# Kernel optimization log

Hardware: AMD Instinct MI355X
Metric: run time of the kernel (lower is better)

The kernel has to match this reference:

```python
import jax, jax.numpy as jnp
from jax import lax
import numpy as np


def _conv(x, w, b, stride=1, pad=0):
    # x: NCHW, w: OIHW
    o = lax.conv_general_dilated(x, w, (stride, stride), [(pad, pad), (pad, pad)],
                                 dimension_numbers=('NCHW', 'OIHW', 'NCHW'))
    return o + b[None, :, None, None]


def _up2(x):
    return jnp.repeat(jnp.repeat(x, 2, axis=2), 2, axis=3)


def _boundary_agg(x, w, b):
    # up_to_bottom = prefix-max along H; bottom_to_up = suffix-max along H;
    # left_to_right / right_to_left (via rot90) = prefix/suffix max along W (square spatial).
    x1 = lax.cummax(x, axis=2)
    x2 = lax.cummax(x, axis=2, reverse=True)
    x3 = lax.cummax(x, axis=3)
    x4 = lax.cummax(x, axis=3, reverse=True)
    return _conv(jnp.concatenate([x, x1, x2, x3, x4], axis=1), w, b)


def _forward(C3, C4, C5,
             ba3_w, ba3_b, ba4_w, ba4_b, ba5_w, ba5_b,
             p5_1_w, p5_1_b, p5_1d_w, p5_1d_b, p5_2_w, p5_2_b,
             p4_1_w, p4_1_b, p4_1d_w, p4_1d_b, p4_2_w, p4_2_b,
             p3_1_w, p3_1_b, p3_1d_w, p3_1d_b, p3_2_w, p3_2_b,
             p6_w, p6_b, p7_w, p7_b,
             c34_w, c34_b, c45_w, c45_b, c35_w, c35_b,
             gamma3, gamma4, gamma5):
    C3_BA = _boundary_agg(C3, ba3_w, ba3_b)
    C4_BA = _boundary_agg(C4, ba4_w, ba4_b)
    C5_BA = _boundary_agg(C5, ba5_w, ba5_b)
    # top-down path
    P5 = _conv(C5, p5_1_w, p5_1_b)
    P5u1 = _up2(P5)
    P5u2 = _up2(P5u1)
    P5 = _conv(P5, p5_2_w, p5_2_b, 1, 1)
    P4 = _conv(C4, p4_1_w, p4_1_b) + P5u1
    P4u1 = _up2(P4)
    P4 = _conv(P4, p4_2_w, p4_2_b, 1, 1)
    P3 = _conv(C3, p3_1_w, p3_1_b) + P4u1 + P5u2
    P3 = _conv(P3, p3_2_w, p3_2_b, 1, 1)
    # bottom-up (dual) path on boundary-aggregated features
    P3d = _conv(C3_BA, p3_1d_w, p3_1d_b)
    P3d1 = _conv(P3d, c34_w, c34_b, 2, 1)   # 3x3 s2 p1
    P3d2 = _conv(P3d1, c35_w, c35_b, 2, 0)  # 2x2 s2 p0
    P4d = _conv(C4_BA, p4_1d_w, p4_1d_b) + P3d1
    P4d1 = _conv(P4d, c45_w, c45_b, 2, 0)   # 2x2 s2 p0
    P5d = _conv(C5_BA, p5_1d_w, p5_1d_b) + P4d1 + P3d2
    # extra levels
    P6 = _conv(C5, p6_w, p6_b, 2, 1)
    P7 = _conv(jax.nn.relu(P6), p7_w, p7_b, 2, 1)
    # gated merge
    O3 = gamma3 * P3d + (1.0 - gamma3) * P3
    O4 = gamma4 * P4d + (1.0 - gamma4) * P4
    O5 = gamma5 * P5d + (1.0 - gamma5) * P5
    return (O3, O4, O5, P6, P7)


def setup_inputs() -> dict:
    key = jax.random.key(0)
    ks = iter(jax.random.split(key, 48))
    def rnd(shape, scale):
        return jax.random.normal(next(ks), shape, dtype=jnp.float32) * scale
    B, F = 8, 256
    d = {
        'C3': rnd((B, 256, 64, 64), 1.0),
        'C4': rnd((B, 512, 32, 32), 1.0),
        'C5': rnd((B, 1024, 16, 16), 1.0),
        # Boundary_Aggregation 1x1 convs: in_channels*5 -> in_channels
        'ba3_w': rnd((256, 1280, 1, 1), 0.02), 'ba3_b': rnd((256,), 0.02),
        'ba4_w': rnd((512, 2560, 1, 1), 0.02), 'ba4_b': rnd((512,), 0.02),
        'ba5_w': rnd((1024, 5120, 1, 1), 0.01), 'ba5_b': rnd((1024,), 0.02),
        # FPN lateral / smoothing convs
        'p5_1_w': rnd((F, 1024, 1, 1), 0.02), 'p5_1_b': rnd((F,), 0.02),
        'p5_1d_w': rnd((F, 1024, 1, 1), 0.02), 'p5_1d_b': rnd((F,), 0.02),
        'p5_2_w': rnd((F, F, 3, 3), 0.02), 'p5_2_b': rnd((F,), 0.02),
        'p4_1_w': rnd((F, 512, 1, 1), 0.02), 'p4_1_b': rnd((F,), 0.02),
        'p4_1d_w': rnd((F, 512, 1, 1), 0.02), 'p4_1d_b': rnd((F,), 0.02),
        'p4_2_w': rnd((F, F, 3, 3), 0.02), 'p4_2_b': rnd((F,), 0.02),
        'p3_1_w': rnd((F, 256, 1, 1), 0.02), 'p3_1_b': rnd((F,), 0.02),
        'p3_1d_w': rnd((F, 256, 1, 1), 0.02), 'p3_1d_b': rnd((F,), 0.02),
        'p3_2_w': rnd((F, F, 3, 3), 0.02), 'p3_2_b': rnd((F,), 0.02),
        'p6_w': rnd((F, 1024, 3, 3), 0.02), 'p6_b': rnd((F,), 0.02),
        'p7_w': rnd((F, F, 3, 3), 0.02), 'p7_b': rnd((F,), 0.02),
        # downsample convs in dual path
        'c34_w': rnd((F, F, 3, 3), 0.02), 'c34_b': rnd((F,), 0.02),
        'c45_w': rnd((F, F, 2, 2), 0.02), 'c45_b': rnd((F,), 0.02),
        'c35_w': rnd((F, F, 2, 2), 0.02), 'c35_b': rnd((F,), 0.02),
        'gamma3': rnd((1,), 0.3), 'gamma4': rnd((1,), 0.3), 'gamma5': rnd((1,), 0.3),
    }
    return d


def reference(C3, C4, C5,
              ba3_w, ba3_b, ba4_w, ba4_b, ba5_w, ba5_b,
              p5_1_w, p5_1_b, p5_1d_w, p5_1d_b, p5_2_w, p5_2_b,
              p4_1_w, p4_1_b, p4_1d_w, p4_1d_b, p4_2_w, p4_2_b,
              p3_1_w, p3_1_b, p3_1d_w, p3_1d_b, p3_2_w, p3_2_b,
              p6_w, p6_b, p7_w, p7_b,
              c34_w, c34_b, c45_w, c45_b, c35_w, c35_b,
              gamma3, gamma4, gamma5):
    return _forward(C3, C4, C5,
                    ba3_w, ba3_b, ba4_w, ba4_b, ba5_w, ba5_b,
                    p5_1_w, p5_1_b, p5_1d_w, p5_1d_b, p5_2_w, p5_2_b,
                    p4_1_w, p4_1_b, p4_1d_w, p4_1d_b, p4_2_w, p4_2_b,
                    p3_1_w, p3_1_b, p3_1d_w, p3_1d_b, p3_2_w, p3_2_b,
                    p6_w, p6_b, p7_w, p7_b,
                    c34_w, c34_b, c45_w, c45_b, c35_w, c35_b,
                    gamma3, gamma4, gamma5)
```

## Files before the change

kernel.cpp:

```cpp
#include <hip/hip_runtime.h>

typedef unsigned short u16;
typedef __attribute__((ext_vector_type(8))) short s8v;
typedef __attribute__((ext_vector_type(4))) float f4v;

__device__ __forceinline__ u16 f2bf(float f) {
  unsigned int x = __float_as_uint(f);
  return (u16)((x + 0x7fffu + ((x >> 16) & 1u)) >> 16);
}
__device__ __forceinline__ float bf2f(u16 u) {
  return __uint_as_float(((unsigned int)u) << 16);
}
__device__ __forceinline__ void gload16(const void* g, void* l) {
  __builtin_amdgcn_global_load_lds(
      (const __attribute__((address_space(1))) void*)g,
      (__attribute__((address_space(3))) void*)l, 16, 0, 0);
}

struct Epi {
  const float* bias;
  const u16* r1; int r1Hp, r1pad, r1sh;
  const u16* r2; int r2Hp, r2pad, r2sh;
  const float* gamma; const u16* other; int oHp, opad, gmode;
  u16* outB; int oBHp, oBpad, oBrelu;
  float* outF;
};

__device__ __forceinline__ size_t nhwc_idx(int b, int h, int w, int Hp, int pad, int Cc, int m) {
  return (((size_t)(b * Hp + h + pad)) * Hp + (w + pad)) * Cc + m;
}

__device__ __forceinline__ f4v epi_val(f4v a, int mbase, int b, int oh, int ow,
                                       float g, const Epi& ep) {
  float v[4];
#pragma unroll
  for (int r = 0; r < 4; ++r) v[r] = a[r];
  if (ep.bias) {
    const float* bp = &ep.bias[mbase];
#pragma unroll
    for (int r = 0; r < 4; ++r) v[r] += bp[r];
  }
  if (ep.r1) {
    const u16* rp = &ep.r1[nhwc_idx(b, oh >> ep.r1sh, ow >> ep.r1sh, ep.r1Hp, ep.r1pad, 256, mbase)];
#pragma unroll
    for (int r = 0; r < 4; ++r) v[r] += bf2f(rp[r]);
  }
  if (ep.r2) {
    const u16* rp = &ep.r2[nhwc_idx(b, oh >> ep.r2sh, ow >> ep.r2sh, ep.r2Hp, ep.r2pad, 256, mbase)];
#pragma unroll
    for (int r = 0; r < 4; ++r) v[r] += bf2f(rp[r]);
  }
  if (ep.gmode) {
    const u16* op = &ep.other[nhwc_idx(b, oh, ow, ep.oHp, ep.opad, 256, mbase)];
#pragma unroll
    for (int r = 0; r < 4; ++r) {
      float o = bf2f(op[r]);
      v[r] = (ep.gmode == 1) ? (g * o + (1.f - g) * v[r]) : (g * v[r] + (1.f - g) * o);
    }
  }
  f4v out;
#pragma unroll
  for (int r = 0; r < 4; ++r) out[r] = v[r];
  return out;
}

__device__ __forceinline__ void epi_storeB(f4v v, int mbase, int b, int oh, int ow,
                                           int M, const Epi& ep) {
  u16* obp = &ep.outB[nhwc_idx(b, oh, ow, ep.oBHp, ep.oBpad, M, mbase)];
  ushort4 pk;
  if (ep.oBrelu) { pk.x = f2bf(fmaxf(v[0], 0.f)); pk.y = f2bf(fmaxf(v[1], 0.f));
                   pk.z = f2bf(fmaxf(v[2], 0.f)); pk.w = f2bf(fmaxf(v[3], 0.f)); }
  else { pk.x = f2bf(v[0]); pk.y = f2bf(v[1]); pk.z = f2bf(v[2]); pk.w = f2bf(v[3]); }
  *(ushort4*)obp = pk;
}

__device__ __forceinline__ void epi4(f4v a, int mbase, int b, int oh, int ow,
                                     int p, int M, int l2ohow, float g, const Epi& ep) {
  f4v v = epi_val(a, mbase, b, oh, ow, g, ep);
  if (ep.outF) {
    float* fp = &ep.outF[(((size_t)(b * M + mbase)) << l2ohow) + p];
#pragma unroll
    for (int r = 0; r < 4; ++r) fp[(size_t)r << l2ohow] = v[r];
  }
  if (ep.outB) epi_storeB(v, mbase, b, oh, ow, M, ep);
}

struct WSeg { const float* src; u16* dst; int K, l2Cin, mode, ktiles, blk0; };
struct WTab { WSeg s[17]; };

__global__ __launch_bounds__(256) void k_cvt_w(WTab tab) {
  int bid = blockIdx.x;
  int si = 0;
#pragma unroll
  for (int i = 1; i < 17; ++i) si += (bid >= tab.s[i].blk0) ? 1 : 0;
  WSeg sg = tab.s[si];
  int rel = bid - sg.blk0;
  int m = rel / sg.ktiles;
  int kt = rel - m * sg.ktiles;
  int r = kt * 256 + threadIdx.x;
  if (r >= sg.K) return;
  int Cin = 1 << sg.l2Cin;
  int q = r >> sg.l2Cin, c = r & (Cin - 1);
  int sidx;
  if (sg.mode == 1) {
    int og = (q < 4) ? (q + 1) : 0;
    sidx = m * sg.K + og * Cin + c;
  } else {
    int KHW = sg.K >> sg.l2Cin;
    sidx = (m * Cin + c) * KHW + q;
  }
  sg.dst[(size_t)m * sg.K + r] = f2bf(sg.src[sidx]);
}

__global__ __launch_bounds__(256) void k_cvt_x(const float* __restrict__ in, u16* __restrict__ out,
                                               int C, int H, int W, int Hp, int P, int tw) {
  __shared__ u16 tile[32][33];
  const int t = threadIdx.x;
  const int b = blockIdx.z, h = blockIdx.y;
  const int tc = blockIdx.x / tw, twi = blockIdx.x - tc * tw;
  const int c0 = tc * 32, w0 = twi * 32;
#pragma unroll
  for (int r = 0; r < 4; ++r) {
    int cl = (t >> 5) * 4 + r, wl = t & 31;
    if (w0 + wl < W) tile[cl][wl] = f2bf(in[(((size_t)b * C + c0 + cl) * H + h) * W + w0 + wl]);
  }
  __syncthreads();
#pragma unroll
  for (int r = 0; r < 4; ++r) {
    int wl = (t >> 5) * 4 + r, cl = t & 31;
    if (w0 + wl < W) out[(((size_t)(b * Hp + h + P)) * Hp + (w0 + wl + P)) * C + c0 + cl] = tile[cl][wl];
  }
}

__global__ __launch_bounds__(256)
void k_scanH(const u16* __restrict__ in, u16* __restrict__ out0, u16* __restrict__ out1,
             int S, int C) {
  const int cpw = C >> 2;
  const int wpb = 256 / cpw;
  const int strips = S / wpb;
  const int t = threadIdx.x;
  const int wl = t / cpw, c4 = t - wl * cpw;
  const int bb = blockIdx.x / strips, strip = blockIdx.x - bb * strips;
  const int w = strip * wpb + wl;
  const size_t hstr = (size_t)S * C;
  const size_t base = (((size_t)bb * S) * S + w) * C + c4 * 4;
  float m0 = -INFINITY, m1 = -INFINITY, m2 = -INFINITY, m3 = -INFINITY;
  if (blockIdx.y == 0) {
    for (int h = 0; h < S; ++h) {
      ushort4 v = *(const ushort4*)&in[base + (size_t)h * hstr];
      m0 = fmaxf(m0, bf2f(v.x)); m1 = fmaxf(m1, bf2f(v.y));
      m2 = fmaxf(m2, bf2f(v.z)); m3 = fmaxf(m3, bf2f(v.w));
      ushort4 o; o.x = f2bf(m0); o.y = f2bf(m1); o.z = f2bf(m2); o.w = f2bf(m3);
      *(ushort4*)&out0[base + (size_t)h * hstr] = o;
    }
  } else {
    for (int h = S - 1; h >= 0; --h) {
      ushort4 v = *(const ushort4*)&in[base + (size_t)h * hstr];
      m0 = fmaxf(m0, bf2f(v.x)); m1 = fmaxf(m1, bf2f(v.y));
      m2 = fmaxf(m2, bf2f(v.z)); m3 = fmaxf(m3, bf2f(v.w));
      ushort4 o; o.x = f2bf(m0); o.y = f2bf(m1); o.z = f2bf(m2); o.w = f2bf(m3);
      *(ushort4*)&out1[base + (size_t)h * hstr] = o;
    }
  }
}

__global__ __launch_bounds__(256)
void k_scanW(const u16* __restrict__ in, u16* __restrict__ out0, u16* __restrict__ out1,
             int S, int C) {
  const int cph = C >> 2;
  const int hpb = 256 / cph;
  const int strips = S / hpb;
  const int t = threadIdx.x;
  const int hl = t / cph, c4 = t - hl * cph;
  const int bb = blockIdx.x / strips, strip = blockIdx.x - bb * strips;
  const int h = strip * hpb + hl;
  const size_t wstr = (size_t)C;
  const size_t base = (((size_t)bb * S + h) * S) * C + c4 * 4;
  float m0 = -INFINITY, m1 = -INFINITY, m2 = -INFINITY, m3 = -INFINITY;
  if (blockIdx.y == 0) {
    for (int w = 0; w < S; ++w) {
      ushort4 v = *(const ushort4*)&in[base + (size_t)w * wstr];
      m0 = fmaxf(m0, bf2f(v.x)); m1 = fmaxf(m1, bf2f(v.y));
      m2 = fmaxf(m2, bf2f(v.z)); m3 = fmaxf(m3, bf2f(v.w));
      ushort4 o; o.x = f2bf(m0); o.y = f2bf(m1); o.z = f2bf(m2); o.w = f2bf(m3);
      *(ushort4*)&out0[base + (size_t)w * wstr] = o;
    }
  } else {
    for (int w = S - 1; w >= 0; --w) {
      ushort4 v = *(const ushort4*)&in[base + (size_t)w * wstr];
      m0 = fmaxf(m0, bf2f(v.x)); m1 = fmaxf(m1, bf2f(v.y));
      m2 = fmaxf(m2, bf2f(v.z)); m3 = fmaxf(m3, bf2f(v.w));
      ushort4 o; o.x = f2bf(m0); o.y = f2bf(m1); o.z = f2bf(m2); o.w = f2bf(m3);
      *(ushort4*)&out1[base + (size_t)w * wstr] = o;
    }
  }
}

template<int QDIV, int KW, int STR, bool FUSE>
__global__ __launch_bounds__(256)
void k_gemm(const u16* __restrict__ X, const u16* __restrict__ X2,
            const u16* __restrict__ Wt,
            float* __restrict__ part, int C, int l2C, int Hp, int ipad,
            int l2ohow, int l2ow, int K, int Ksp, int M, int N, Epi ep) {
  __shared__ __align__(16) u16 SMEM[FUSE ? 12288 : 17408];
  u16* Al = SMEM;
  u16* Bl = SMEM + 4096;
  float* Cl = (float*)SMEM;
  const int tid = threadIdx.x, lane = tid & 63, wid = tid >> 6;

  int ntile, mtile;
  {
    const int NT = gridDim.x, MT = gridDim.y;
    int nm = blockIdx.x + NT * blockIdx.y;
    if ((NT & 7) == 0) {
      int low = nm & 7, r = nm >> 3;
      mtile = r % MT;
      ntile = ((r / MT) << 3) + low;
    } else { ntile = blockIdx.x; mtile = blockIdx.y; }
  }
  const int n0 = ntile * 128, m0 = mtile * 64;
  const int kb = blockIdx.z * Ksp;
  const int mw = (wid >> 1) * 32, nw = (wid & 1) * 64;

  const int srow = lane >> 2;
  const int schunk = (lane & 3) ^ ((srow >> 1) & 3);

  const u16* pa0 = Wt + (size_t)(m0 + wid * 16 + srow) * K + kb + schunk * 8;

  const u16* pb0 = nullptr; const u16* pb1 = nullptr;
  int rowB[2], ohsB[2], owsB[2];
  int q = 0, cnt = 0, khs = 0, kws = 0;
#pragma unroll
  for (int j = 0; j < 2; ++j) {
    int n = n0 + wid * 32 + j * 16 + srow;
    int b = n >> l2ohow, p = n & ((1 << l2ohow) - 1);
    int oh = p >> l2ow, ow = p & ((1 << l2ow) - 1);
    if (QDIV == 1) {
      const u16* gg = X + ((size_t)(b * Hp + oh + ipad) * Hp + (ow + ipad)) * C + kb + schunk * 8;
      if (j == 0) pb0 = gg; else pb1 = gg;
    } else if (QDIV == 5) {
      rowB[j] = n;
    } else {
      rowB[j] = b * Hp; ohsB[j] = oh * STR + ipad; owsB[j] = ow * STR + ipad;
    }
  }
  if (QDIV == 5) {
    q = kb >> l2C;
    int c0 = kb & (C - 1);
    cnt = (C - c0) >> 5;
    const u16* base = (q < 4) ? (X + (((size_t)q << Hp) << l2C)) : X2;
    pb0 = base + (((size_t)rowB[0]) << l2C) + c0 + schunk * 8;
    pb1 = base + (((size_t)rowB[1]) << l2C) + c0 + schunk * 8;
  } else if (QDIV != 1) {
    q = kb >> l2C;
    int c0 = kb & (C - 1);
    cnt = (C - c0) >> 5;
    if (QDIV == 4) { khs = q >> 1; kws = q & 1; } else { khs = q / 3; kws = q - khs * 3; }
    pb0 = X + ((size_t)(rowB[0] + ohsB[0] + khs) * Hp + (owsB[0] + kws)) * C + c0 + schunk * 8;
    pb1 = X + ((size_t)(rowB[1] + ohsB[1] + khs) * Hp + (owsB[1] + kws)) * C + c0 + schunk * 8;
  }

  f4v acc[2][4];
#pragma unroll
  for (int i = 0; i < 2; ++i)
#pragma unroll
    for (int j = 0; j < 4; ++j) acc[i][j] = (f4v){0.f, 0.f, 0.f, 0.f};

  const int fr = lane & 15, kc = lane >> 4;
  const int fxor = (kc ^ ((fr >> 1) & 3)) * 8;

  auto advB = [&]() {
    if (QDIV == 1) { pb0 += 32; pb1 += 32; }
    else if (--cnt == 0) {
      ++q; cnt = C >> 5;
      if (QDIV == 5) {
        const u16* base = (q < 4) ? (X + (((size_t)q << Hp) << l2C)) : X2;
        pb0 = base + (((size_t)rowB[0]) << l2C) + schunk * 8;
        pb1 = base + (((size_t)rowB[1]) << l2C) + schunk * 8;
      } else {
        if (++kws == KW) { kws = 0; ++khs; }
        pb0 = X + ((size_t)(rowB[0] + ohsB[0] + khs) * Hp + (owsB[0] + kws)) * C + schunk * 8;
        pb1 = X + ((size_t)(rowB[1] + ohsB[1] + khs) * Hp + (owsB[1] + kws)) * C + schunk * 8;
      }
    } else { pb0 += 32; pb1 += 32; }
  };
  auto stage = [&](int buf) {
    u16* la = Al + buf * 2048 + wid * 512;
    u16* lb = Bl + buf * 4096 + wid * 1024;
    gload16(pa0, la);
    gload16(pb0, lb); gload16(pb1, lb + 512);
    pa0 += 32;
    advB();
  };

  const int nt = Ksp >> 5;
  stage(0);
  for (int t = 0; t < nt; ++t) {
    const int cur = t & 1;
    if (t + 1 < nt) {
      stage(cur ^ 1);
      asm volatile("s_waitcnt vmcnt(3)" ::: "memory");
    } else {
      asm volatile("s_waitcnt vmcnt(0)" ::: "memory");
    }
    __builtin_amdgcn_s_barrier();
    asm volatile("" ::: "memory");
    const u16* ca = Al + cur * 2048;
    const u16* cb = Bl + cur * 4096;
    s8v a[2], bv[4];
#pragma unroll
    for (int mf = 0; mf < 2; ++mf) a[mf] = *(const s8v*)&ca[(mw + mf * 16 + fr) * 32 + fxor];
#pragma unroll
    for (int nf = 0; nf < 4; ++nf) bv[nf] = *(const s8v*)&cb[(nw + nf * 16 + fr) * 32 + fxor];
#pragma unroll
    for (int mf = 0; mf < 2; ++mf)
#pragma unroll
      for (int nf = 0; nf < 4; ++nf)
        acc[mf][nf] = __builtin_amdgcn_mfma_f32_16x16x32_bf16(a[mf], bv[nf], acc[mf][nf], 0, 0, 0);
    __builtin_amdgcn_s_barrier();
    asm volatile("" ::: "memory");
  }

  const int r4 = kc * 4;
  if (FUSE) {
    float g = ep.gmode ? *ep.gamma : 0.f;
#pragma unroll
    for (int nf = 0; nf < 4; ++nf) {
      int n = n0 + nw + nf * 16 + fr;
      int b = n >> l2ohow, p = n & ((1 << l2ohow) - 1);
      int oh = p >> l2ow, ow = p & ((1 << l2ow) - 1);
#pragma unroll
      for (int mf = 0; mf < 2; ++mf)
        epi4(acc[mf][nf], m0 + mw + mf * 16 + r4, b, oh, ow, p, M, l2ohow, g, ep);
    }
  } else {
#pragma unroll
    for (int nf = 0; nf < 4; ++nf) {
      int pl = nw + nf * 16 + fr;
#pragma unroll
      for (int mf = 0; mf < 2; ++mf)
        *(f4v*)&Cl[pl * 68 + mw + mf * 16 + r4] = acc[mf][nf];
    }
    __builtin_amdgcn_s_barrier();
    asm volatile("" ::: "memory");
    const int ml2 = (tid & 15) << 2;
    const int prow = tid >> 4;
#pragma unroll
    for (int pass = 0; pass < 8; ++pass) {
      int pl = pass * 16 + prow;
      int n = n0 + pl;
      *(f4v*)&part[((size_t)blockIdx.z * N + n) * M + m0 + ml2] =
          *(const f4v*)&Cl[pl * 68 + ml2];
    }
  }
}

__global__ __launch_bounds__(256)
void k_red2(const float* __restrict__ part, int z, int l2N, int l2M4, int M,
            int l2ohow, int l2ow, Epi ep) {
  const size_t total = (size_t)1 << (l2N + l2M4);
  const int N = 1 << l2N;
  float g = ep.gmode ? *ep.gamma : 0.f;
  for (size_t t = (size_t)blockIdx.x * 256 + threadIdx.x; t < total;
       t += (size_t)gridDim.x * 256) {
    int m4 = (int)(t & ((1u << l2M4) - 1));
    int n = (int)(t >> l2M4);
    int m = m4 << 2;
    f4v v = (f4v){0.f, 0.f, 0.f, 0.f};
    for (int s = 0; s < z; ++s) {
      f4v x = *(const f4v*)&part[((size_t)s * N + n) * M + m];
      v = v + x;
    }
    int b = n >> l2ohow, p = n & ((1 << l2ohow) - 1);
    int oh = p >> l2ow, ow = p & ((1 << l2ow) - 1);
    epi4(v, m, b, oh, ow, p, M, l2ohow, g, ep);
  }
}

static const size_t WR_BA3 = 0, WR_BA4 = 327680, WR_BA5 = 1638400,
  WR_P51 = 6881280, WR_P51D = 7143424, WR_P52 = 7405568, WR_P41 = 7995392,
  WR_P41D = 8126464, WR_P42 = 8257536, WR_P31 = 8847360, WR_P31D = 8912896,
  WR_P32 = 8978432, WR_P6 = 9568256, WR_P7 = 11927552, WR_C34 = 12517376,
  WR_C45 = 13107200, WR_C35 = 13369344;
static const size_t O_C3N = 13631488, O_C4N = 22020096, O_C5N = 26214400,
  O_C3BA = 28311552, O_C4BA = 36700160, O_C5BA = 40894464,
  O_CAT = 42991616, O_SCR = 76546048;
static const size_t O_P3D = O_CAT, O_P3PRE = O_CAT + 8921088,
  O_P4PRE = O_CAT + 17842176, O_P3D1 = O_CAT + 20209664,
  O_P4D = O_CAT + 22306816, O_P4D1 = O_CAT + 24403968,
  O_P3D2 = O_CAT + 24928256, O_P5PRE = O_CAT + 25452544,
  O_P5S = O_CAT + 26116096, O_P6R = O_CAT + 26640384, O_C5P = O_CAT + 26845184;

extern "C" void kernel_launch(void* const* d_in, const int* in_sizes, int n_in,
                              void* d_out, int out_size, void* d_ws, size_t ws_size,
                              hipStream_t stream) {
  (void)in_sizes; (void)n_in; (void)out_size; (void)ws_size;
  const float* C3 = (const float*)d_in[0];
  const float* C4 = (const float*)d_in[1];
  const float* C5 = (const float*)d_in[2];
  const float* ba3_w = (const float*)d_in[3];  const float* ba3_b = (const float*)d_in[4];
  const float* ba4_w = (const float*)d_in[5];  const float* ba4_b = (const float*)d_in[6];
  const float* ba5_w = (const float*)d_in[7];  const float* ba5_b = (const float*)d_in[8];
  const float* p5_1_w = (const float*)d_in[9];  const float* p5_1_b = (const float*)d_in[10];
  const float* p5_1d_w = (const float*)d_in[11]; const float* p5_1d_b = (const float*)d_in[12];
  const float* p5_2_w = (const float*)d_in[13]; const float* p5_2_b = (const float*)d_in[14];
  const float* p4_1_w = (const float*)d_in[15]; const float* p4_1_b = (const float*)d_in[16];
  const float* p4_1d_w = (const float*)d_in[17]; const float* p4_1d_b = (const float*)d_in[18];
  const float* p4_2_w = (const float*)d_in[19]; const float* p4_2_b = (const float*)d_in[20];
  const float* p3_1_w = (const float*)d_in[21]; const float* p3_1_b = (const float*)d_in[22];
  const float* p3_1d_w = (const float*)d_in[23]; const float* p3_1d_b = (const float*)d_in[24];
  const float* p3_2_w = (const float*)d_in[25]; const float* p3_2_b = (const float*)d_in[26];
  const float* p6_w = (const float*)d_in[27]; const float* p6_b = (const float*)d_in[28];
  const float* p7_w = (const float*)d_in[29]; const float* p7_b = (const float*)d_in[30];
  const float* c34_w = (const float*)d_in[31]; const float* c34_b = (const float*)d_in[32];
  const float* c45_w = (const float*)d_in[33]; const float* c45_b = (const float*)d_in[34];
  const float* c35_w = (const float*)d_in[35]; const float* c35_b = (const float*)d_in[36];
  const float* g3 = (const float*)d_in[37];
  const float* g4 = (const float*)d_in[38];
  const float* g5 = (const float*)d_in[39];

  float* out = (float*)d_out;
  float* O3 = out;
  float* O4 = out + 8388608;
  float* O5 = out + 10485760;
  float* P6o = out + 11010048;
  float* P7o = out + 11141120;

  u16* wsu = (u16*)d_ws;
  u16* c3n = wsu + O_C3N;  u16* c4n = wsu + O_C4N;  u16* c5n = wsu + O_C5N;
  u16* c3ba = wsu + O_C3BA; u16* c4ba = wsu + O_C4BA; u16* c5ba = wsu + O_C5BA;
  u16* catb = wsu + O_CAT;
  u16* scr = wsu + O_SCR;
  u16* p3d = wsu + O_P3D;  u16* p3d1 = wsu + O_P3D1; u16* p3d2 = wsu + O_P3D2;
  u16* p4d = wsu + O_P4D;  u16* p4d1 = wsu + O_P4D1;
  u16* p5pre = wsu + O_P5PRE; u16* p5s = wsu + O_P5S; u16* p4pre = wsu + O_P4PRE;
  u16* p3pre = wsu + O_P3PRE; u16* p6r = wsu + O_P6R; u16* c5p = wsu + O_C5P;
  float* part = (float*)scr;
  float* partba = (float*)scr;

  const Epi enone = {nullptr, nullptr,0,0,0, nullptr,0,0,0, nullptr,nullptr,0,0,0, nullptr,0,0,0, nullptr};

  WTab tab;
  int ti = 0, blk = 0;
  auto add = [&](const float* s, size_t off, int M, int K, int l2Cin, int mode) {
    int kt = (K + 255) / 256;
    tab.s[ti].src = s; tab.s[ti].dst = wsu + off; tab.s[ti].K = K;
    tab.s[ti].l2Cin = l2Cin; tab.s[ti].mode = mode;
    tab.s[ti].ktiles = kt; tab.s[ti].blk0 = blk;
    blk += M * kt; ++ti;
  };
  add(ba3_w, WR_BA3, 256, 1280, 8, 1);
  add(ba4_w, WR_BA4, 512, 2560, 9, 1);
  add(ba5_w, WR_BA5, 1024, 5120, 10, 1);
  add(p5_1_w, WR_P51, 256, 1024, 10, 0);
  add(p5_1d_w, WR_P51D, 256, 1024, 10, 0);
  add(p5_2_w, WR_P52, 256, 2304, 8, 0);
  add(p4_1_w, WR_P41, 256, 512, 9, 0);
  add(p4_1d_w, WR_P41D, 256, 512, 9, 0);
  add(p4_2_w, WR_P42, 256, 2304, 8, 0);
  add(p3_1_w, WR_P31, 256, 256, 8, 0);
  add(p3_1d_w, WR_P31D, 256, 256, 8, 0);
  add(p3_2_w, WR_P32, 256, 2304, 8, 0);
  add(p6_w, WR_P6, 256, 9216, 10, 0);
  add(p7_w, WR_P7, 256, 2304, 8, 0);
  add(c34_w, WR_C34, 256, 2304, 8, 0);
  add(c45_w, WR_C45, 256, 1024, 8, 0);
  add(c35_w, WR_C35, 256, 1024, 8, 0);
  k_cvt_w<<<blk, 256, 0, stream>>>(tab);

  k_cvt_x<<<dim3(16,64,8), 256, 0, stream>>>(C3, c3n, 256, 64, 64, 64, 0, 2);
  k_cvt_x<<<dim3(16,32,8), 256, 0, stream>>>(C4, c4n, 512, 32, 32, 32, 0, 1);
  k_cvt_x<<<dim3(32,16,8), 256, 0, stream>>>(C5, c5n, 1024, 16, 16, 16, 0, 1);

  {
    const size_t GS3 = 8388608;
    k_scanH<<<dim3(128,2), 256, 0, stream>>>(c3n, catb, catb + GS3, 64, 256);
    k_scanW<<<dim3(128,2), 256, 0, stream>>>(c3n, catb + 2*GS3, catb + 3*GS3, 64, 256);
    Epi ep = {ba3_b, nullptr,0,0,0, nullptr,0,0,0, nullptr,nullptr,0,0,0, c3ba,64,0,0, nullptr};
    k_gemm<5,1,1,true><<<dim3(256,4,1), 256, 0, stream>>>(
        catb, c3n, wsu + WR_BA3, nullptr, 256, 8, 15, 0, 12, 6, 1280, 1280, 256, 32768, ep);
  }
  {
    const size_t GS4 = 4194304;
    k_scanH<<<dim3(128,2), 256, 0, stream>>>(c4n, catb, catb + GS4, 32, 512);
    k_scanW<<<dim3(128,2), 256, 0, stream>>>(c4n, catb + 2*GS4, catb + 3*GS4, 32, 512);
    k_gemm<5,1,1,false><<<dim3(64,8,2), 256, 0, stream>>>(
        catb, c4n, wsu + WR_BA4, partba, 512, 9, 13, 0, 10, 5, 2560, 1280, 512, 8192, enone);
    Epi ep = {ba4_b, nullptr,0,0,0, nullptr,0,0,0, nullptr,nullptr,0,0,0, c4ba,32,0,0, nullptr};
    k_red2<<<2048, 256, 0, stream>>>(partba, 2, 13, 7, 512, 10, 5, ep);
  }
  {
    const size_t GS5 = 2097152;
    k_scanH<<<dim3(128,2), 256, 0, stream>>>(c5n, catb, catb + GS5, 16, 1024);
    k_scanW<<<dim3(128,2), 256, 0, stream>>>(c5n, catb + 2*GS5, catb + 3*GS5, 16, 1024);
    k_gemm<5,1,1,false><<<dim3(16,16,4), 256, 0, stream>>>(
        catb, c5n, wsu + WR_BA5, partba, 1024, 10, 11, 0, 8, 4, 5120, 1280, 1024, 2048, enone);
    Epi ep = {ba5_b, nullptr,0,0,0, nullptr,0,0,0, nullptr,nullptr,0,0,0, c5ba,16,0,0, nullptr};
    k_red2<<<2048, 256, 0, stream>>>(partba, 4, 11, 8, 1024, 8, 4, ep);
  }

  hipMemsetAsync(p3d, 0, (size_t)8921088 * 2, stream);
  hipMemsetAsync(p3pre, 0, (size_t)8921088 * 2, stream);
  hipMemsetAsync(p4pre, 0, (size_t)2367488 * 2, stream);
  hipMemsetAsync(p5pre, 0, (size_t)663552 * 2, stream);
  hipMemsetAsync(p6r, 0, (size_t)204800 * 2, stream);
  hipMemsetAsync(c5p, 0, (size_t)2654208 * 2, stream);
  k_cvt_x<<<dim3(32,16,8), 256, 0, stream>>>(C5, c5p, 1024, 16, 16, 18, 1, 1);

  {
    Epi ep = {p3_1d_b, nullptr,0,0,0, nullptr,0,0,0, nullptr,nullptr,0,0,0, p3d,66,1,0, nullptr};
    k_gemm<1,1,1,true><<<dim3(256,4,1), 256, 0, stream>>>(
        c3ba, nullptr, wsu + WR_P31D, nullptr, 256, 0, 64, 0, 12, 6, 256, 256, 256, 32768, ep);
  }
  k_gemm<9,3,2,false><<<dim3(64,4,4), 256, 0, stream>>>(
      p3d, nullptr, wsu + WR_C34, part, 256, 8, 66, 0, 10, 5, 2304, 576, 256, 8192, enone);
  {
    Epi ep = {c34_b, nullptr,0,0,0, nullptr,0,0,0, nullptr,nullptr,0,0,0, p3d1,32,0,0, nullptr};
    k_red2<<<2048, 256, 0, stream>>>(part, 4, 13, 6, 256, 10, 5, ep);
  }
  k_gemm<4,2,2,false><<<dim3(16,4,8), 256, 0, stream>>>(
      p3d1, nullptr, wsu + WR_C35, part, 256, 8, 32, 0, 8, 4, 1024, 128, 256, 2048, enone);
  {
    Epi ep = {c35_b, nullptr,0,0,0, nullptr,0,0,0, nullptr,nullptr,0,0,0, p3d2,16,0,0, nullptr};
    k_red2<<<2048, 256, 0, stream>>>(part, 8, 11, 6, 256, 8, 4, ep);
  }
  k_gemm<1,1,1,false><<<dim3(64,4,4), 256, 0, stream>>>(
      c4ba, nullptr, wsu + WR_P41D, part, 512, 0, 32, 0, 10, 5, 512, 128, 256, 8192, enone);
  {
    Epi ep = {p4_1d_b, p3d1,32,0,0, nullptr,0,0,0, nullptr,nullptr,0,0,0, p4d,32,0,0, nullptr};
    k_red2<<<2048, 256, 0, stream>>>(part, 4, 13, 6, 256, 10, 5, ep);
  }
  k_gemm<4,2,2,false><<<dim3(16,4,8), 256, 0, stream>>>(
      p4d, nullptr, wsu + WR_C45, part, 256, 8, 32, 0, 8, 4, 1024, 128, 256, 2048, enone);
  {
    Epi ep = {c45_b, nullptr,0,0,0, nullptr,0,0,0, nullptr,nullptr,0,0,0, p4d1,16,0,0, nullptr};
    k_red2<<<2048, 256, 0, stream>>>(part, 8, 11, 6, 256, 8, 4, ep);
  }

  k_gemm<1,1,1,false><<<dim3(16,4,8), 256, 0, stream>>>(
      c5n, nullptr, wsu + WR_P51, part, 1024, 0, 16, 0, 8, 4, 1024, 128, 256, 2048, enone);
  {
    Epi ep = {p5_1_b, nullptr,0,0,0, nullptr,0,0,0, nullptr,nullptr,0,0,0, p5pre,18,1,0, nullptr};
    k_red2<<<2048, 256, 0, stream>>>(part, 8, 11, 6, 256, 8, 4, ep);
  }
  k_gemm<9,3,1,false><<<dim3(16,4,8), 256, 0, stream>>>(
      p5pre, nullptr, wsu + WR_P52, part, 256, 8, 18, 0, 8, 4, 2304, 288, 256, 2048, enone);
  {
    Epi ep = {p5_2_b, nullptr,0,0,0, nullptr,0,0,0, nullptr,nullptr,0,0,0, p5s,16,0,0, nullptr};
    k_red2<<<2048, 256, 0, stream>>>(part, 8, 11, 6, 256, 8, 4, ep);
  }
  k_gemm<1,1,1,false><<<dim3(64,4,4), 256, 0, stream>>>(
      c4n, nullptr, wsu + WR_P41, part, 512, 0, 32, 0, 10, 5, 512, 128, 256, 8192, enone);
  {
    Epi ep = {p4_1_b, p5pre,18,1,1, nullptr,0,0,0, nullptr,nullptr,0,0,0, p4pre,34,1,0, nullptr};
    k_red2<<<2048, 256, 0, stream>>>(part, 4, 13, 6, 256, 10, 5, ep);
  }
  k_gemm<9,3,1,false><<<dim3(64,4,4), 256, 0, stream>>>(
      p4pre, nullptr, wsu + WR_P42, part, 256, 8, 34, 0, 10, 5, 2304, 576, 256, 8192, enone);
  {
    Epi ep = {p4_2_b, nullptr,0,0,0, nullptr,0,0,0, g4,p4d,32,0,1, nullptr,0,0,0, O4};
    k_red2<<<2048, 256, 0, stream>>>(part, 4, 13, 6, 256, 10, 5, ep);
  }
  {
    Epi ep = {p3_1_b, p4pre,34,1,1, p5pre,18,1,2, nullptr,nullptr,0,0,0, p3pre,66,1,0, nullptr};
    k_gemm<1,1,1,true><<<dim3(256,4,1), 256, 0, stream>>>(
        c3n, nullptr, wsu + WR_P31, nullptr, 256, 0, 64, 0, 12, 6, 256, 256, 256, 32768, ep);
  }
  {
    Epi ep = {p3_2_b, nullptr,0,0,0, nullptr,0,0,0, g3,p3d,66,1,1, nullptr,0,0,0, O3};
    k_gemm<9,3,1,true><<<dim3(256,4,1), 256, 0, stream>>>(
        p3pre, nullptr, wsu + WR_P32, nullptr, 256, 8, 66, 0, 12, 6, 2304, 2304, 256, 32768, ep);
  }
  k_gemm<1,1,1,false><<<dim3(16,4,8), 256, 0, stream>>>(
      c5ba, nullptr, wsu + WR_P51D, part, 1024, 0, 16, 0, 8, 4, 1024, 128, 256, 2048, enone);
  {
    Epi ep = {p5_1d_b, p4d1,16,0,0, p3d2,16,0,0, g5,p5s,16,0,2, nullptr,0,0,0, O5};
    k_red2<<<2048, 256, 0, stream>>>(part, 8, 11, 6, 256, 8, 4, ep);
  }

  k_gemm<9,3,2,false><<<dim3(4,4,32), 256, 0, stream>>>(
      c5p, nullptr, wsu + WR_P6, part, 1024, 10, 18, 0, 6, 3, 9216, 288, 256, 512, enone);
  {
    Epi ep = {p6_b, nullptr,0,0,0, nullptr,0,0,0, nullptr,nullptr,0,0,0, p6r,10,1,1, P6o};
    k_red2<<<512, 256, 0, stream>>>(part, 32, 9, 6, 256, 6, 3, ep);
  }
  k_gemm<9,3,2,false><<<dim3(1,4,8), 256, 0, stream>>>(
      p6r, nullptr, wsu + WR_P7, part, 256, 8, 10, 0, 4, 2, 2304, 288, 256, 128, enone);
  {
    Epi ep = {p7_b, nullptr,0,0,0, nullptr,0,0,0, nullptr,nullptr,0,0,0, nullptr,0,0,0, P7o};
    k_red2<<<128, 256, 0, stream>>>(part, 8, 7, 6, 256, 4, 2, ep);
  }
}
```

Before: 654.6 us.

## Add LDS-free register-pipelined GEMM kernel for fused-epilogue convolutions

Introduces k_gemmf, which loads A and B fragments straight from global memory into registers with a four-stage software pipeline, skipping LDS staging and barriers. It is used for the four large fused-epilogue GEMMs (the level-3 boundary-agg conv, the P3d and P3 1x1 convs, and the P3 3x3 conv). The aim is to remove LDS traffic and barrier stalls on these grids. The cost is many uncoalesced 16-byte global loads per lane with no data sharing between warps, plus higher register pressure. The FUSE path is removed from k_gemm.

```diff
diff --git a/kernel.cpp b/kernel.cpp
--- a/kernel.cpp
+++ b/kernel.cpp
@@ -196,13 +196,143 @@
   }
 }
 
-template<int QDIV, int KW, int STR, bool FUSE>
+#define LSET(A0v,A1v,B0v,B1v,B2v,B3v) \
+    A0v = *(const s8v*)pa0; A1v = *(const s8v*)pa1; \
+    B0v = *(const s8v*)pb0; B1v = *(const s8v*)pb1; \
+    B2v = *(const s8v*)pb2; B3v = *(const s8v*)pb3; \
+    pa0 += 32; pa1 += 32; advB();
+#define MSET(A0v,A1v,B0v,B1v,B2v,B3v) \
+    acc[0][0] = __builtin_amdgcn_mfma_f32_16x16x32_bf16(A0v, B0v, acc[0][0], 0, 0, 0); \
+    acc[0][1] = __builtin_amdgcn_mfma_f32_16x16x32_bf16(A0v, B1v, acc[0][1], 0, 0, 0); \
+    acc[0][2] = __builtin_amdgcn_mfma_f32_16x16x32_bf16(A0v, B2v, acc[0][2], 0, 0, 0); \
+    acc[0][3] = __builtin_amdgcn_mfma_f32_16x16x32_bf16(A0v, B3v, acc[0][3], 0, 0, 0); \
+    acc[1][0] = __builtin_amdgcn_mfma_f32_16x16x32_bf16(A1v, B0v, acc[1][0], 0, 0, 0); \
+    acc[1][1] = __builtin_amdgcn_mfma_f32_16x16x32_bf16(A1v, B1v, acc[1][1], 0, 0, 0); \
+    acc[1][2] = __builtin_amdgcn_mfma_f32_16x16x32_bf16(A1v, B2v, acc[1][2], 0, 0, 0); \
+    acc[1][3] = __builtin_amdgcn_mfma_f32_16x16x32_bf16(A1v, B3v, acc[1][3], 0, 0, 0);
+
+template<int QDIV, int KW, int STR>
+__global__ __launch_bounds__(256)
+void k_gemmf(const u16* __restrict__ X, const u16* __restrict__ X2,
+             const u16* __restrict__ Wt,
+             int C, int l2C, int Hp, int ipad,
+             int l2ohow, int l2ow, int K, int M, int N, Epi ep) {
+  const int tid = threadIdx.x, lane = tid & 63, wid = tid >> 6;
+
+  int ntile, mtile;
+  {
+    const int NT = gridDim.x, MT = gridDim.y;
+    int nm = blockIdx.x + NT * blockIdx.y;
+    if ((NT & 7) == 0) {
+      int low = nm & 7, r = nm >> 3;
+      mtile = r % MT;
+      ntile = ((r / MT) << 3) + low;
+    } else { ntile = blockIdx.x; mtile = blockIdx.y; }
+  }
+  const int n0 = ntile * 128, m0 = mtile * 64;
+  const int mw = (wid >> 1) * 32, nw = (wid & 1) * 64;
+  const int fr = lane & 15, kc = lane >> 4;
+
+  const u16* pa0 = Wt + (size_t)(m0 + mw + fr) * K + kc * 8;
+  const u16* pa1 = pa0 + (size_t)16 * K;
+
+  const u16* pb0; const u16* pb1; const u16* pb2; const u16* pb3;
+  int rowB[4], ohsB[4], owsB[4];
+  int q = 0, cnt = 0, khs = 0, kws = 0;
+#pragma unroll
+  for (int nf = 0; nf < 4; ++nf) {
+    int n = n0 + nw + nf * 16 + fr;
+    int b = n >> l2ohow, p = n & ((1 << l2ohow) - 1);
+    int oh = p >> l2ow, ow = p & ((1 << l2ow) - 1);
+    if (QDIV == 1) {
+      const u16* gg = X + ((size_t)(b * Hp + oh + ipad) * Hp + (ow + ipad)) * C + kc * 8;
+      if (nf == 0) pb0 = gg; else if (nf == 1) pb1 = gg; else if (nf == 2) pb2 = gg; else pb3 = gg;
+    } else if (QDIV == 5) {
+      rowB[nf] = n;
+    } else {
+      rowB[nf] = b * Hp; ohsB[nf] = oh * STR + ipad; owsB[nf] = ow * STR + ipad;
+    }
+  }
+  if (QDIV == 5) {
+    cnt = C >> 5;
+    pb0 = X + (((size_t)rowB[0]) << l2C) + kc * 8;
+    pb1 = X + (((size_t)rowB[1]) << l2C) + kc * 8;
+    pb2 = X + (((size_t)rowB[2]) << l2C) + kc * 8;
+    pb3 = X + (((size_t)rowB[3]) << l2C) + kc * 8;
+  } else if (QDIV != 1) {
+    cnt = C >> 5;
+    pb0 = X + ((size_t)(rowB[0] + ohsB[0]) * Hp + owsB[0]) * C + kc * 8;
+    pb1 = X + ((size_t)(rowB[1] + ohsB[1]) * Hp + owsB[1]) * C + kc * 8;
+    pb2 = X + ((size_t)(rowB[2] + ohsB[2]) * Hp + owsB[2]) * C + kc * 8;
+    pb3 = X + ((size_t)(rowB[3] + ohsB[3]) * Hp + owsB[3]) * C + kc * 8;
+  }
+
+  f4v acc[2][4];
+#pragma unroll
+  for (int i = 0; i < 2; ++i)
+#pragma unroll
+    for (int j = 0; j < 4; ++j) acc[i][j] = (f4v){0.f, 0.f, 0.f, 0.f};
+
+  auto advB = [&]() {
+    if (QDIV == 1) { pb0 += 32; pb1 += 32; pb2 += 32; pb3 += 32; }
+    else if (--cnt == 0) {
+      ++q; cnt = C >> 5;
+      if (QDIV == 5) {
+        const u16* base = (q < 4) ? (X + (((size_t)q << Hp) << l2C)) : X2;
+        pb0 = base + (((size_t)rowB[0]) << l2C) + kc * 8;
+        pb1 = base + (((size_t)rowB[1]) << l2C) + kc * 8;
+        pb2 = base + (((size_t)rowB[2]) << l2C) + kc * 8;
+        pb3 = base + (((size_t)rowB[3]) << l2C) + kc * 8;
+      } else {
+        if (++kws == KW) { kws = 0; ++khs; }
+        pb0 = X + ((size_t)(rowB[0] + ohsB[0] + khs) * Hp + (owsB[0] + kws)) * C + kc * 8;
+        pb1 = X + ((size_t)(rowB[1] + ohsB[1] + khs) * Hp + (owsB[1] + kws)) * C + kc * 8;
+        pb2 = X + ((size_t)(rowB[2] + ohsB[2] + khs) * Hp + (owsB[2] + kws)) * C + kc * 8;
+        pb3 = X + ((size_t)(rowB[3] + ohsB[3] + khs) * Hp + (owsB[3] + kws)) * C + kc * 8;
+      }
+    } else { pb0 += 32; pb1 += 32; pb2 += 32; pb3 += 32; }
+  };
+
+  const int nt = K >> 5;
+  s8v a00, a01, b00, b01, b02, b03;
+  s8v a10, a11, b10, b11, b12, b13;
+  s8v a20, a21, b20, b21, b22, b23;
+  s8v a30, a31, b30, b31, b32, b33;
+  LSET(a00, a01, b00, b01, b02, b03)
+  LSET(a10, a11, b10, b11, b12, b13)
+  LSET(a20, a21, b20, b21, b22, b23)
+  LSET(a30, a31, b30, b31, b32, b33)
+  for (int t = 0; t < nt; t += 4) {
+    MSET(a00, a01, b00, b01, b02, b03)
+    if (t + 4 < nt) { LSET(a00, a01, b00, b01, b02, b03) }
+    MSET(a10, a11, b10, b11, b12, b13)
+    if (t + 5 < nt) { LSET(a10, a11, b10, b11, b12, b13) }
+    MSET(a20, a21, b20, b21, b22, b23)
+    if (t + 6 < nt) { LSET(a20, a21, b20, b21, b22, b23) }
+    MSET(a30, a31, b30, b31, b32, b33)
+    if (t + 7 < nt) { LSET(a30, a31, b30, b31, b32, b33) }
+  }
+
+  const int r4 = kc * 4;
+  float g = ep.gmode ? *ep.gamma : 0.f;
+#pragma unroll
+  for (int nf = 0; nf < 4; ++nf) {
+    int n = n0 + nw + nf * 16 + fr;
+    int b = n >> l2ohow, p = n & ((1 << l2ohow) - 1);
+    int oh = p >> l2ow, ow = p & ((1 << l2ow) - 1);
+#pragma unroll
+    for (int mf = 0; mf < 2; ++mf)
+      epi4(acc[mf][nf], m0 + mw + mf * 16 + r4, b, oh, ow, p, M, l2ohow, g, ep);
+  }
+}
+
+template<int QDIV, int KW, int STR>
 __global__ __launch_bounds__(256)
 void k_gemm(const u16* __restrict__ X, const u16* __restrict__ X2,
             const u16* __restrict__ Wt,
             float* __restrict__ part, int C, int l2C, int Hp, int ipad,
             int l2ohow, int l2ow, int K, int Ksp, int M, int N, Epi ep) {
-  __shared__ __align__(16) u16 SMEM[FUSE ? 12288 : 17408];
+  __shared__ __align__(16) u16 SMEM[17408];
   u16* Al = SMEM;
   u16* Bl = SMEM + 4096;
   float* Cl = (float*)SMEM;
@@ -322,36 +452,23 @@
   }
 
   const int r4 = kc * 4;
-  if (FUSE) {
-    float g = ep.gmode ? *ep.gamma : 0.f;
-#pragma unroll
-    for (int nf = 0; nf < 4; ++nf) {
-      int n = n0 + nw + nf * 16 + fr;
-      int b = n >> l2ohow, p = n & ((1 << l2ohow) - 1);
-      int oh = p >> l2ow, ow = p & ((1 << l2ow) - 1);
-#pragma unroll
-      for (int mf = 0; mf < 2; ++mf)
-        epi4(acc[mf][nf], m0 + mw + mf * 16 + r4, b, oh, ow, p, M, l2ohow, g, ep);
-    }
-  } else {
-#pragma unroll
-    for (int nf = 0; nf < 4; ++nf) {
-      int pl = nw + nf * 16 + fr;
-#pragma unroll
-      for (int mf = 0; mf < 2; ++mf)
-        *(f4v*)&Cl[pl * 68 + mw + mf * 16 + r4] = acc[mf][nf];
-    }
-    __builtin_amdgcn_s_barrier();
-    asm volatile("" ::: "memory");
-    const int ml2 = (tid & 15) << 2;
-    const int prow = tid >> 4;
-#pragma unroll
-    for (int pass = 0; pass < 8; ++pass) {
-      int pl = pass * 16 + prow;
-      int n = n0 + pl;
-      *(f4v*)&part[((size_t)blockIdx.z * N + n) * M + m0 + ml2] =
-          *(const f4v*)&Cl[pl * 68 + ml2];
-    }
+#pragma unroll
+  for (int nf = 0; nf < 4; ++nf) {
+    int pl = nw + nf * 16 + fr;
+#pragma unroll
+    for (int mf = 0; mf < 2; ++mf)
+      *(f4v*)&Cl[pl * 68 + mw + mf * 16 + r4] = acc[mf][nf];
+  }
+  __builtin_amdgcn_s_barrier();
+  asm volatile("" ::: "memory");
+  const int ml2 = (tid & 15) << 2;
+  const int prow = tid >> 4;
+#pragma unroll
+  for (int pass = 0; pass < 8; ++pass) {
+    int pl = pass * 16 + prow;
+    int n = n0 + pl;
+    *(f4v*)&part[((size_t)blockIdx.z * N + n) * M + m0 + ml2] =
+        *(const f4v*)&Cl[pl * 68 + ml2];
   }
 }
 
@@ -477,14 +594,14 @@
     k_scanH<<<dim3(128,2), 256, 0, stream>>>(c3n, catb, catb + GS3, 64, 256);
     k_scanW<<<dim3(128,2), 256, 0, stream>>>(c3n, catb + 2*GS3, catb + 3*GS3, 64, 256);
     Epi ep = {ba3_b, nullptr,0,0,0, nullptr,0,0,0, nullptr,nullptr,0,0,0, c3ba,64,0,0, nullptr};
-    k_gemm<5,1,1,true><<<dim3(256,4,1), 256, 0, stream>>>(
-        catb, c3n, wsu + WR_BA3, nullptr, 256, 8, 15, 0, 12, 6, 1280, 1280, 256, 32768, ep);
+    k_gemmf<5,1,1><<<dim3(256,4,1), 256, 0, stream>>>(
+        catb, c3n, wsu + WR_BA3, 256, 8, 15, 0, 12, 6, 1280, 256, 32768, ep);
   }
   {
     const size_t GS4 = 4194304;
     k_scanH<<<dim3(128,2), 256, 0, stream>>>(c4n, catb, catb + GS4, 32, 512);
     k_scanW<<<dim3(128,2), 256, 0, stream>>>(c4n, catb + 2*GS4, catb + 3*GS4, 32, 512);
-    k_gemm<5,1,1,false><<<dim3(64,8,2), 256, 0, stream>>>(
+    k_gemm<5,1,1><<<dim3(64,8,2), 256, 0, stream>>>(
         catb, c4n, wsu + WR_BA4, partba, 512, 9, 13, 0, 10, 5, 2560, 1280, 512, 8192, enone);
     Epi ep = {ba4_b, nullptr,0,0,0, nullptr,0,0,0, nullptr,nullptr,0,0,0, c4ba,32,0,0, nullptr};
     k_red2<<<2048, 256, 0, stream>>>(partba, 2, 13, 7, 512, 10, 5, ep);
@@ -493,7 +610,7 @@
     const size_t GS5 = 2097152;
     k_scanH<<<dim3(128,2), 256, 0, stream>>>(c5n, catb, catb + GS5, 16, 1024);
     k_scanW<<<dim3(128,2), 256, 0, stream>>>(c5n, catb + 2*GS5, catb + 3*GS5, 16, 1024);
-    k_gemm<5,1,1,false><<<dim3(16,16,4), 256, 0, stream>>>(
+    k_gemm<5,1,1><<<dim3(16,16,4), 256, 0, stream>>>(
         catb, c5n, wsu + WR_BA5, partba, 1024, 10, 11, 0, 8, 4, 5120, 1280, 1024, 2048, enone);
     Epi ep = {ba5_b, nullptr,0,0,0, nullptr,0,0,0, nullptr,nullptr,0,0,0, c5ba,16,0,0, nullptr};
     k_red2<<<2048, 256, 0, stream>>>(partba, 4, 11, 8, 1024, 8, 4, ep);
@@ -509,53 +626,53 @@
 
   {
     Epi ep = {p3_1d_b, nullptr,0,0,0, nullptr,0,0,0, nullptr,nullptr,0,0,0, p3d,66,1,0, nullptr};
-    k_gemm<1,1,1,true><<<dim3(256,4,1), 256, 0, stream>>>(
-        c3ba, nullptr, wsu + WR_P31D, nullptr, 256, 0, 64, 0, 12, 6, 256, 256, 256, 32768, ep);
-  }
-  k_gemm<9,3,2,false><<<dim3(64,4,4), 256, 0, stream>>>(
+    k_gemmf<1,1,1><<<dim3(256,4,1), 256, 0, stream>>>(
+        c3ba, nullptr, wsu + WR_P31D, 256, 0, 64, 0, 12, 6, 256, 256, 32768, ep);
+  }
+  k_gemm<9,3,2><<<dim3(64,4,4), 256, 0, stream>>>(
       p3d, nullptr, wsu + WR_C34, part, 256, 8, 66, 0, 10, 5, 2304, 576, 256, 8192, enone);
   {
     Epi ep = {c34_b, nullptr,0,0,0, nullptr,0,0,0, nullptr,nullptr,0,0,0, p3d1,32,0,0, nullptr};
     k_red2<<<2048, 256, 0, stream>>>(part, 4, 13, 6, 256, 10, 5, ep);
   }
-  k_gemm<4,2,2,false><<<dim3(16,4,8), 256, 0, stream>>>(
+  k_gemm<4,2,2><<<dim3(16,4,8), 256, 0, stream>>>(
       p3d1, nullptr, wsu + WR_C35, part, 256, 8, 32, 0, 8, 4, 1024, 128, 256, 2048, enone);
   {
     Epi ep = {c35_b, nullptr,0,0,0, nullptr,0,0,0, nullptr,nullptr,0,0,0, p3d2,16,0,0, nullptr};
     k_red2<<<2048, 256, 0, stream>>>(part, 8, 11, 6, 256, 8, 4, ep);
   }
-  k_gemm<1,1,1,false><<<dim3(64,4,4), 256, 0, stream>>>(
+  k_gemm<1,1,1><<<dim3(64,4,4), 256, 0, stream>>>(
       c4ba, nullptr, wsu + WR_P41D, part, 512, 0, 32, 0, 10, 5, 512, 128, 256, 8192, enone);
   {
     Epi ep = {p4_1d_b, p3d1,32,0,0, nullptr,0,0,0, nullptr,nullptr,0,0,0, p4d,32,0,0, nullptr};
     k_red2<<<2048, 256, 0, stream>>>(part, 4, 13, 6, 256, 10, 5, ep);
   }
-  k_gemm<4,2,2,false><<<dim3(16,4,8), 256, 0, stream>>>(
+  k_gemm<4,2,2><<<dim3(16,4,8), 256, 0, stream>>>(
       p4d, nullptr, wsu + WR_C45, part, 256, 8, 32, 0, 8, 4, 1024, 128, 256, 2048, enone);
   {
     Epi ep = {c45_b, nullptr,0,0,0, nullptr,0,0,0, nullptr,nullptr,0,0,0, p4d1,16,0,0, nullptr};
     k_red2<<<2048, 256, 0, stream>>>(part, 8, 11, 6, 256, 8, 4, ep);
   }
 
-  k_gemm<1,1,1,false><<<dim3(16,4,8), 256, 0, stream>>>(
+  k_gemm<1,1,1><<<dim3(16,4,8), 256, 0, stream>>>(
       c5n, nullptr, wsu + WR_P51, part, 1024, 0, 16, 0, 8, 4, 1024, 128, 256, 2048, enone);
   {
     Epi ep = {p5_1_b, nullptr,0,0,0, nullptr,0,0,0, nullptr,nullptr,0,0,0, p5pre,18,1,0, nullptr};
     k_red2<<<2048, 256, 0, stream>>>(part, 8, 11, 6, 256, 8, 4, ep);
   }
-  k_gemm<9,3,1,false><<<dim3(16,4,8), 256, 0, stream>>>(
+  k_gemm<9,3,1><<<dim3(16,4,8), 256, 0, stream>>>(
       p5pre, nullptr, wsu + WR_P52, part, 256, 8, 18, 0, 8, 4, 2304, 288, 256, 2048, enone);
   {
     Epi ep = {p5_2_b, nullptr,0,0,0, nullptr,0,0,0, nullptr,nullptr,0,0,0, p5s,16,0,0, nullptr};
     k_red2<<<2048, 256, 0, stream>>>(part, 8, 11, 6, 256, 8, 4, ep);
   }
-  k_gemm<1,1,1,false><<<dim3(64,4,4), 256, 0, stream>>>(
+  k_gemm<1,1,1><<<dim3(64,4,4), 256, 0, stream>>>(
       c4n, nullptr, wsu + WR_P41, part, 512, 0, 32, 0, 10, 5, 512, 128, 256, 8192, enone);
   {
     Epi ep = {p4_1_b, p5pre,18,1,1, nullptr,0,0,0, nullptr,nullptr,0,0,0, p4pre,34,1,0, nullptr};
     k_red2<<<2048, 256, 0, stream>>>(part, 4, 13, 6, 256, 10, 5, ep);
   }
-  k_gemm<9,3,1,false><<<dim3(64,4,4), 256, 0, stream>>>(
+  k_gemm<9,3,1><<<dim3(64,4,4), 256, 0, stream>>>(
       p4pre, nullptr, wsu + WR_P42, part, 256, 8, 34, 0, 10, 5, 2304, 576, 256, 8192, enone);
   {
     Epi ep = {p4_2_b, nullptr,0,0,0, nullptr,0,0,0, g4,p4d,32,0,1, nullptr,0,0,0, O4};
@@ -563,28 +680,28 @@
   }
   {
     Epi ep = {p3_1_b, p4pre,34,1,1, p5pre,18,1,2, nullptr,nullptr,0,0,0, p3pre,66,1,0, nullptr};
-    k_gemm<1,1,1,true><<<dim3(256,4,1), 256, 0, stream>>>(
-        c3n, nullptr, wsu + WR_P31, nullptr, 256, 0, 64, 0, 12, 6, 256, 256, 256, 32768, ep);
+    k_gemmf<1,1,1><<<dim3(256,4,1), 256, 0, stream>>>(
+        c3n, nullptr, wsu + WR_P31, 256, 0, 64, 0, 12, 6, 256, 256, 32768, ep);
   }
   {
     Epi ep = {p3_2_b, nullptr,0,0,0, nullptr,0,0,0, g3,p3d,66,1,1, nullptr,0,0,0, O3};
-    k_gemm<9,3,1,true><<<dim3(256,4,1), 256, 0, stream>>>(
-        p3pre, nullptr, wsu + WR_P32, nullptr, 256, 8, 66, 0, 12, 6, 2304, 2304, 256, 32768, ep);
-  }
-  k_gemm<1,1,1,false><<<dim3(16,4,8), 256, 0, stream>>>(
+    k_gemmf<9,3,1><<<dim3(256,4,1), 256, 0, stream>>>(
+        p3pre, nullptr, wsu + WR_P32, 256, 8, 66, 0, 12, 6, 2304, 256, 32768, ep);
+  }
+  k_gemm<1,1,1><<<dim3(16,4,8), 256, 0, stream>>>(
       c5ba, nullptr, wsu + WR_P51D, part, 1024, 0, 16, 0, 8, 4, 1024, 128, 256, 2048, enone);
   {
     Epi ep = {p5_1d_b, p4d1,16,0,0, p3d2,16,0,0, g5,p5s,16,0,2, nullptr,0,0,0, O5};
     k_red2<<<2048, 256, 0, stream>>>(part, 8, 11, 6, 256, 8, 4, ep);
   }
 
-  k_gemm<9,3,2,false><<<dim3(4,4,32), 256, 0, stream>>>(
+  k_gemm<9,3,2><<<dim3(4,4,32), 256, 0, stream>>>(
       c5p, nullptr, wsu + WR_P6, part, 1024, 10, 18, 0, 6, 3, 9216, 288, 256, 512, enone);
   {
     Epi ep = {p6_b, nullptr,0,0,0, nullptr,0,0,0, nullptr,nullptr,0,0,0, p6r,10,1,1, P6o};
     k_red2<<<512, 256, 0, stream>>>(part, 32, 9, 6, 256, 6, 3, ep);
   }
-  k_gemm<9,3,2,false><<<dim3(1,4,8), 256, 0, stream>>>(
+  k_gemm<9,3,2><<<dim3(1,4,8), 256, 0, stream>>>(
       p6r, nullptr, wsu + WR_P7, part, 256, 8, 10, 0, 4, 2, 2304, 288, 256, 128, enone);
   {
     Epi ep = {p7_b, nullptr,0,0,0, nullptr,0,0,0, nullptr,nullptr,0,0,0, nullptr,0,0,0, P7o};
```

Result: slower. 898.7 us (+37.3%).
